# Kernel optimization log

Hardware: AMD Instinct MI355X
Metric: run time of the kernel (lower is better)

Reference implementation:

```python
import jax, jax.numpy as jnp
import numpy as np

N, E, G = 25000, 50000, 1000   # nodes, edges, graphs
NP, EP = 25, 50                # nodes/edges per graph
D = 64                         # node_out_feats


def setup_inputs() -> dict:
    key = jax.random.key(0)
    ks = jax.random.split(key, 32)
    rng = np.random.RandomState(0)
    # edges stay within their graph (molecular batch structure)
    base = np.repeat(np.arange(G), EP) * NP
    src = jnp.asarray(base + rng.randint(0, NP, E), dtype=jnp.int32)
    dst = jnp.asarray(base + rng.randint(0, NP, E), dtype=jnp.int32)
    graph_ids = jnp.repeat(jnp.arange(G, dtype=jnp.int32), NP)

    def p(i, shape, s=0.05):
        return (jax.random.normal(ks[i], shape, jnp.float32) * s)

    return dict(
        n_feats=jax.random.normal(ks[0], (N, 74), jnp.float32),
        e_feats=jax.random.normal(ks[1], (E, 12), jnp.float32),
        src=src, dst=dst, graph_ids=graph_ids,
        # project_node_feats: Linear(74,64)+ReLU
        proj_W=p(2, (74, D)), proj_b=jnp.zeros((D,), jnp.float32),
        # NNConv edge network: Linear(12,64)+ReLU+Linear(64,64*64)
        eW1=p(3, (12, D)), eb1=jnp.zeros((D,), jnp.float32),
        eW2=p(4, (D, D * D)), eb2=jnp.zeros((D * D,), jnp.float32),
        conv_b=jnp.zeros((D,), jnp.float32),
        # GRU (1 layer, gates r,z,n) stored transposed: x @ W
        gru_Wi=p(5, (D, 3 * D)), gru_Wh=p(6, (D, 3 * D)),
        gru_bi=jnp.zeros((3 * D,), jnp.float32), gru_bh=jnp.zeros((3 * D,), jnp.float32),
        # Set2Set LSTM: 3 layers, input 2D (layer0) / D, hidden D, gates i,f,g,o
        lWi0=p(7, (2 * D, 4 * D)), lWh0=p(8, (D, 4 * D)), lb0=jnp.zeros((4 * D,), jnp.float32),
        lWi1=p(9, (D, 4 * D)), lWh1=p(10, (D, 4 * D)), lb1=jnp.zeros((4 * D,), jnp.float32),
        lWi2=p(11, (D, 4 * D)), lWh2=p(12, (D, 4 * D)), lb2=jnp.zeros((4 * D,), jnp.float32),
        # predict hidden: Linear(128,64)+ReLU, then head fc: Linear(64,1)
        pW=p(13, (2 * D, D)), pb=jnp.zeros((D,), jnp.float32),
        fW=p(14, (D, 1)), fb=jnp.zeros((1,), jnp.float32),
    )


def reference(n_feats, e_feats, src, dst, graph_ids,
              proj_W, proj_b, eW1, eb1, eW2, eb2, conv_b,
              gru_Wi, gru_Wh, gru_bi, gru_bh,
              lWi0, lWh0, lb0, lWi1, lWh1, lb1, lWi2, lWh2, lb2,
              pW, pb, fW, fb):
    # --- MPNNGNN ---
    h = jax.nn.relu(n_feats @ proj_W + proj_b)                      # (N, D)
    W_e = (jax.nn.relu(e_feats @ eW1 + eb1) @ eW2 + eb2).reshape(E, D, D)
    g = h                                                            # GRU hidden init = node feats
    for _ in range(3):
        msg = jnp.einsum('ei,eio->eo', h[src], W_e)                  # per-edge message
        m = jax.nn.relu(jax.ops.segment_sum(msg, dst, num_segments=N) + conv_b)
        gi = m @ gru_Wi + gru_bi
        gh = g @ gru_Wh + gru_bh
        ir, iz, inn = jnp.split(gi, 3, -1)
        hr, hz, hn = jnp.split(gh, 3, -1)
        r = jax.nn.sigmoid(ir + hr)
        z = jax.nn.sigmoid(iz + hz)
        nn_ = jnp.tanh(inn + r * hn)
        g = (1.0 - z) * nn_ + z * g
        h = g
    # --- Set2Set readout (3 iters, 3-layer LSTM) ---
    Wis, Whs, bs = [lWi0, lWi1, lWi2], [lWh0, lWh1, lWh2], [lb0, lb1, lb2]
    hs = [jnp.zeros((G, D), h.dtype) for _ in range(3)]
    cs = [jnp.zeros((G, D), h.dtype) for _ in range(3)]
    q_star = jnp.zeros((G, 2 * D), h.dtype)
    for _ in range(3):
        x = q_star
        for l in range(3):
            gates = x @ Wis[l] + hs[l] @ Whs[l] + bs[l]
            i, f, gg, o = jnp.split(gates, 4, -1)
            cs[l] = jax.nn.sigmoid(f) * cs[l] + jax.nn.sigmoid(i) * jnp.tanh(gg)
            hs[l] = jax.nn.sigmoid(o) * jnp.tanh(cs[l])
            x = hs[l]
        q = x                                                        # (G, D)
        e = jnp.sum(h * q[graph_ids], -1)                            # (N,)
        e = e - jax.ops.segment_max(e, graph_ids, num_segments=G)[graph_ids]
        ex = jnp.exp(e)
        alpha = ex / jax.ops.segment_sum(ex, graph_ids, num_segments=G)[graph_ids]
        rdt = jax.ops.segment_sum(alpha[:, None] * h, graph_ids, num_segments=G)
        q_star = jnp.concatenate([q, rdt], -1)                       # (G, 2D)
    # --- predict hidden + head ---
    graph_feats = jax.nn.relu(q_star @ pW + pb)                      # (G, D)
    return jax.nn.sigmoid(graph_feats @ fW + fb)[:, 0]               # (G,)
```

## Files before the change

kernel.cpp:

```cpp
#include <hip/hip_runtime.h>
#include <math.h>

__device__ __forceinline__ float sigf(float x) { return 1.f / (1.f + expf(-x)); }

using half8v = __attribute__((ext_vector_type(8))) _Float16;
using f32x4  = __attribute__((ext_vector_type(4))) float;

__device__ __forceinline__ unsigned short f2h(float x) {
    union { _Float16 h; unsigned short u; } c; c.h = (_Float16)x; return c.u;
}
__device__ __forceinline__ half8v u2h(uint4 v) {
    union { uint4 u; half8v h; } c; c.u = v; return c.h;
}

template<int K, int MODE>
__global__ __launch_bounds__(256, 4)
void rowmat_relu_t(const float* __restrict__ in, const float* __restrict__ W,
                   const float* __restrict__ b, float* __restrict__ out32,
                   _Float16* __restrict__ out16, int R)
{
    __shared__ float Wl[K * 64];
    __shared__ float rowsS[32 * K];

    const int tid  = threadIdx.x;
    const int row0 = blockIdx.x * 32;

    for (int i = tid; i < K * 64; i += 256)
        Wl[i] = W[i];
    const int lim = (R - row0 >= 32 ? 32 : (R - row0)) * K;
    for (int i = tid; i < 32 * K; i += 256)
        rowsS[i] = (i < lim) ? in[(size_t)row0 * K + i] : 0.f;
    __syncthreads();

    const int wave = tid >> 6, lane = tid & 63;
    const float bv = b[lane];

    float acc[8];
    #pragma unroll
    for (int rr = 0; rr < 8; ++rr) acc[rr] = bv;

    #pragma unroll 2
    for (int k = 0; k < K; ++k) {
        const float wv = Wl[k * 64 + lane];
        #pragma unroll
        for (int rr = 0; rr < 8; ++rr)
            acc[rr] = fmaf(rowsS[(wave * 8 + rr) * K + k], wv, acc[rr]);
    }

    #pragma unroll
    for (int rr = 0; rr < 8; ++rr) {
        const int row = row0 + wave * 8 + rr;
        if (row < R) {
            const float v = fmaxf(acc[rr], 0.f);
            if (MODE == 0) out32[(size_t)row * 64 + lane] = v;
            out16[(size_t)row * 64 + lane] = (_Float16)v;
        }
    }
}

__global__ __launch_bounds__(256)
void prep_w_kernel(const float* __restrict__ eW2, const float* __restrict__ eb2,
                   unsigned short* __restrict__ w_staged)
{
    int slot = blockIdx.x * 256 + threadIdx.x;
    if (slot >= 65 * 512) return;
    int kc   = slot >> 9;
    int s    = slot & 511;
    int sub  = s >> 6, lane = s & 63;
    int wn   = sub >> 2, tn = (sub >> 1) & 1, ks = sub & 1;
    int kg   = lane >> 4, l15 = lane & 15;
    int o    = wn * 32 + tn * 16 + l15;
    int seg  = kg + ks * 4;
    int j0   = kc * 64 + seg * 8;
    unsigned int packed[4];
    #pragma unroll
    for (int p = 0; p < 4; ++p) {
        int j = j0 + p * 2;
        float v0 = (j     < 4096) ? eW2[(size_t)j * 64 + o]       : eb2[(size_t)(j - 4096) * 64 + o];
        float v1 = (j + 1 < 4096) ? eW2[(size_t)(j + 1) * 64 + o] : eb2[(size_t)(j + 1 - 4096) * 64 + o];
        packed[p] = (unsigned int)f2h(v0) | ((unsigned int)f2h(v1) << 16);
    }
    uint4 st = {packed[0], packed[1], packed[2], packed[3]};
    ((uint4*)w_staged)[slot] = st;
}

__global__ __launch_bounds__(256)
void prep_gruw_kernel(const float* __restrict__ Wi, const float* __restrict__ Wh,
                      _Float16* __restrict__ WiT, _Float16* __restrict__ WhT)
{
    int idx = blockIdx.x * 256 + threadIdx.x;
    if (idx >= 2 * 12288) return;
    const float* W = (idx < 12288) ? Wi : Wh;
    _Float16*    O = (idx < 12288) ? WiT : WhT;
    int r = idx & 12287;
    int n = r >> 6, k = r & 63;
    O[n * 64 + k] = (_Float16)W[(size_t)k * 192 + n];
}

__global__ __launch_bounds__(256)
void prep_s2sw_kernel(const float* __restrict__ lWi0, const float* __restrict__ lWh0,
                      const float* __restrict__ lWi1, const float* __restrict__ lWh1,
                      const float* __restrict__ lWi2, const float* __restrict__ lWh2,
                      _Float16* __restrict__ WB0, _Float16* __restrict__ WB1,
                      _Float16* __restrict__ WB2)
{
    int idx = blockIdx.x * 256 + threadIdx.x;
    if (idx < 49152) {
        int k = idx >> 8, n = idx & 255;
        float v = (k < 128) ? lWi0[(size_t)k * 256 + n] : lWh0[(size_t)(k - 128) * 256 + n];
        WB0[((k >> 3) * 2048) + n * 8 + (k & 7)] = (_Float16)v;
    } else if (idx < 81920) {
        int r = idx - 49152;
        int k = r >> 8, n = r & 255;
        float v = (k < 64) ? lWi1[(size_t)k * 256 + n] : lWh1[(size_t)(k - 64) * 256 + n];
        WB1[((k >> 3) * 2048) + n * 8 + (k & 7)] = (_Float16)v;
    } else if (idx < 114688) {
        int r = idx - 81920;
        int k = r >> 8, n = r & 255;
        float v = (k < 64) ? lWi2[(size_t)k * 256 + n] : lWh2[(size_t)(k - 64) * 256 + n];
        WB2[((k >> 3) * 2048) + n * 8 + (k & 7)] = (_Float16)v;
    }
}

__global__ __launch_bounds__(512, 4)
void msg_mfma_kernel(const _Float16* __restrict__ t16, const _Float16* __restrict__ h16,
                     const int* __restrict__ src, const int* __restrict__ dst,
                     const unsigned short* __restrict__ w_staged,
                     float* __restrict__ msum, int E)
{
    __shared__ _Float16 tS[64 * 134];

    const int tid  = threadIdx.x;
    const int lane = tid & 63;
    const int wave = tid >> 6;
    const int wn   = wave & 1;
    const int wm   = wave >> 1;
    const int e0   = blockIdx.x * 128;

    #pragma unroll
    for (int p = 0; p < 2; ++p) {
        int slot = tid + p * 512;
        int e = slot >> 3, k0 = (slot & 7) * 8;
        int ee = e0 + e;
        half8v tv8 = (half8v)(_Float16)0.f;
        if (ee < E) tv8 = ((const half8v*)(t16 + (size_t)ee * 64))[slot & 7];
        #pragma unroll
        for (int j = 0; j < 8; ++j)
            tS[(k0 + j) * 134 + e] = tv8[j];
    }

    const int l15 = lane & 15;
    const int kg  = lane >> 4;

    half8v Hh[2][2];
    #pragma unroll
    for (int tm = 0; tm < 2; ++tm) {
        const int edge = e0 + wm * 32 + tm * 16 + l15;
        const int sidx = (edge < E) ? src[edge] : 0;
        const half8v* hp = (const half8v*)(h16 + (size_t)sidx * 64);
        Hh[tm][0] = hp[kg];
        Hh[tm][1] = hp[kg + 4];
    }

    const uint4* W4  = (const uint4*)w_staged;
    const int    wb  = wn * 256 + lane;

    uint4 S0a, S0b, S0c, S0d, S1a, S1b, S1c, S1d;
    uint4 S2a, S2b, S2c, S2d, S3a, S3b, S3c, S3d;

#define LOADC(A, B, C, D, cc)                                         \
    { size_t off = (size_t)(cc) * 512 + wb;                           \
      A = W4[off]; B = W4[off + 64]; C = W4[off + 128]; D = W4[off + 192]; }

#define COMP(A, B, C, D, TV0, TV1)                                            \
    { half8v af00 = Hh[0][0] * (TV0), af01 = Hh[0][1] * (TV0);                \
      half8v af10 = Hh[1][0] * (TV1), af11 = Hh[1][1] * (TV1);                \
      half8v b00 = u2h(A), b01 = u2h(B), b10 = u2h(C), b11 = u2h(D);          \
      acc00 = __builtin_amdgcn_mfma_f32_16x16x32_f16(af00, b00, acc00, 0,0,0);\
      acc01 = __builtin_amdgcn_mfma_f32_16x16x32_f16(af00, b10, acc01, 0,0,0);\
      acc10 = __builtin_amdgcn_mfma_f32_16x16x32_f16(af10, b00, acc10, 0,0,0);\
      acc11 = __builtin_amdgcn_mfma_f32_16x16x32_f16(af10, b10, acc11, 0,0,0);\
      acc00 = __builtin_amdgcn_mfma_f32_16x16x32_f16(af01, b01, acc00, 0,0,0);\
      acc01 = __builtin_amdgcn_mfma_f32_16x16x32_f16(af01, b11, acc01, 0,0,0);\
      acc10 = __builtin_amdgcn_mfma_f32_16x16x32_f16(af11, b01, acc10, 0,0,0);\
      acc11 = __builtin_amdgcn_mfma_f32_16x16x32_f16(af11, b11, acc11, 0,0,0); }

    LOADC(S0a, S0b, S0c, S0d, 0)
    LOADC(S1a, S1b, S1c, S1d, 1)
    LOADC(S2a, S2b, S2c, S2d, 2)
    LOADC(S3a, S3b, S3c, S3d, 3)

    f32x4 acc00, acc01, acc10, acc11;
    #pragma unroll
    for (int j = 0; j < 4; ++j) { acc00[j] = 0.f; acc01[j] = 0.f; acc10[j] = 0.f; acc11[j] = 0.f; }

    __syncthreads();

    const int tvb0 = wm * 32 + l15, tvb1 = wm * 32 + 16 + l15;

    for (int c = 0; c < 64; c += 4) {
        _Float16 ta0 = tS[(c + 0) * 134 + tvb0], tb0 = tS[(c + 0) * 134 + tvb1];
        _Float16 ta1 = tS[(c + 1) * 134 + tvb0], tb1 = tS[(c + 1) * 134 + tvb1];
        _Float16 ta2 = tS[(c + 2) * 134 + tvb0], tb2 = tS[(c + 2) * 134 + tvb1];
        _Float16 ta3 = tS[(c + 3) * 134 + tvb0], tb3 = tS[(c + 3) * 134 + tvb1];

        COMP(S0a, S0b, S0c, S0d, ta0, tb0)
        if (c + 4 <= 64) LOADC(S0a, S0b, S0c, S0d, c + 4)
        COMP(S1a, S1b, S1c, S1d, ta1, tb1)
        if (c + 5 <= 64) LOADC(S1a, S1b, S1c, S1d, c + 5)
        COMP(S2a, S2b, S2c, S2d, ta2, tb2)
        if (c + 6 <= 64) LOADC(S2a, S2b, S2c, S2d, c + 6)
        COMP(S3a, S3b, S3c, S3d, ta3, tb3)
        if (c + 7 <= 64) LOADC(S3a, S3b, S3c, S3d, c + 7)
    }
    {
        const _Float16 one = (_Float16)1.0f;
        COMP(S0a, S0b, S0c, S0d, one, one)
    }
#undef LOADC
#undef COMP

    f32x4 acc[2][2] = {{acc00, acc01}, {acc10, acc11}};
    #pragma unroll
    for (int tm = 0; tm < 2; ++tm) {
        #pragma unroll
        for (int j = 0; j < 4; ++j) {
            const int edge = e0 + wm * 32 + tm * 16 + kg * 4 + j;
            if (edge >= E) continue;
            const int d = dst[edge];
            #pragma unroll
            for (int tn = 0; tn < 2; ++tn)
                atomicAdd(&msum[(size_t)d * 64 + wn * 32 + tn * 16 + l15], acc[tm][tn][j]);
        }
    }
}

__global__ __launch_bounds__(256, 2)
void gru_mfma_kernel(const float* __restrict__ msum, float* __restrict__ h,
                     _Float16* __restrict__ h16,
                     const _Float16* __restrict__ WiT, const _Float16* __restrict__ WhT,
                     const float* __restrict__ bi, const float* __restrict__ bh,
                     const float* __restrict__ conv_b, int N)
{
    __shared__ _Float16 BtI[192 * 72];
    __shared__ _Float16 BtH[192 * 72];
    __shared__ _Float16 Am[64 * 72];
    __shared__ _Float16 Ah[64 * 72];

    const int tid  = threadIdx.x;
    const int lane = tid & 63;
    const int wave = tid >> 6;
    const int m0   = wave * 16;
    const int row0 = blockIdx.x * 64;

    #pragma unroll
    for (int p = 0; p < 6; ++p) {
        int slot = tid + p * 256;
        int n = slot >> 3, k0 = (slot & 7) * 8;
        uint4 vi = ((const uint4*)WiT)[slot];
        uint4 vh = ((const uint4*)WhT)[slot];
        *(uint4*)&BtI[n * 72 + k0] = vi;
        *(uint4*)&BtH[n * 72 + k0] = vh;
    }
    #pragma unroll
    for (int p = 0; p < 4; ++p) {
        int idx = tid + p * 256;
        int r = idx >> 4, k4 = (idx & 15) * 4;
        int row = row0 + r;
        float4 mv = make_float4(0.f, 0.f, 0.f, 0.f);
        if (row < N) mv = *(const float4*)&msum[(size_t)row * 64 + k4];
        float4 cb = *(const float4*)&conv_b[k4];
        union { _Float16 hx[4]; uint2 u2; } pk;
        pk.hx[0] = (_Float16)fmaxf(mv.x + cb.x, 0.f);
        pk.hx[1] = (_Float16)fmaxf(mv.y + cb.y, 0.f);
        pk.hx[2] = (_Float16)fmaxf(mv.z + cb.z, 0.f);
        pk.hx[3] = (_Float16)fmaxf(mv.w + cb.w, 0.f);
        *(uint2*)&Am[r * 72 + k4] = pk.u2;
    }
    #pragma unroll
    for (int p = 0; p < 2; ++p) {
        int idx = tid + p * 256;
        int r = idx >> 3, k0 = (idx & 7) * 8;
        int row = row0 + r;
        uint4 v = {0u, 0u, 0u, 0u};
        if (row < N) v = *(const uint4*)&h16[(size_t)row * 64 + k0];
        *(uint4*)&Ah[r * 72 + k0] = v;
    }
    __syncthreads();

    const int l15 = lane & 15;

    f32x4 acc_i[12], acc_h[12];
    #pragma unroll
    for (int nt = 0; nt < 12; ++nt) {
        #pragma unroll
        for (int j = 0; j < 4; ++j) { acc_i[nt][j] = 0.f; acc_h[nt][j] = 0.f; }
    }

    #pragma unroll
    for (int ks = 0; ks < 2; ++ks) {
        const int ka = ks * 32 + (lane >> 4) * 8;
        half8v am = *(const half8v*)&Am[(m0 + l15) * 72 + ka];
        half8v ah = *(const half8v*)&Ah[(m0 + l15) * 72 + ka];
        #pragma unroll
        for (int nt = 0; nt < 12; ++nt) {
            half8v b_i = *(const half8v*)&BtI[(nt * 16 + l15) * 72 + ka];
            half8v b_h = *(const half8v*)&BtH[(nt * 16 + l15) * 72 + ka];
            acc_i[nt] = __builtin_amdgcn_mfma_f32_16x16x32_f16(am, b_i, acc_i[nt], 0, 0, 0);
            acc_h[nt] = __builtin_amdgcn_mfma_f32_16x16x32_f16(ah, b_h, acc_h[nt], 0, 0, 0);
        }
    }

    const int rgrp = lane >> 4;
    #pragma unroll
    for (int nt0 = 0; nt0 < 4; ++nt0) {
        const int c = nt0 * 16 + l15;
        const float bir = bi[c],        bhr = bh[c];
        const float biz = bi[64 + c],   bhz = bh[64 + c];
        const float bin = bi[128 + c],  bhn = bh[128 + c];
        #pragma unroll
        for (int j = 0; j < 4; ++j) {
            const int row = row0 + m0 + rgrp * 4 + j;
            if (row >= N) continue;
            float rg = sigf(acc_i[nt0][j]      + bir + acc_h[nt0][j]      + bhr);
            float zg = sigf(acc_i[4 + nt0][j]  + biz + acc_h[4 + nt0][j]  + bhz);
            float ng = tanhf(acc_i[8 + nt0][j] + bin + rg * (acc_h[8 + nt0][j] + bhn));
            float hold = h[(size_t)row * 64 + c];
            float hv = (1.f - zg) * ng + zg * hold;
            h[(size_t)row * 64 + c]   = hv;
            h16[(size_t)row * 64 + c] = (_Float16)hv;
        }
    }
}

__device__ __forceinline__ float gate_dot8(const _Float16* __restrict__ WB,
                                           int tid, const float* __restrict__ xs,
                                           int nblk)
{
    float a0 = 0.f, a1 = 0.f, a2 = 0.f, a3 = 0.f;
    #pragma unroll 4
    for (int b = 0; b < nblk; ++b) {
        half8v w = *(const half8v*)(WB + (size_t)b * 2048 + tid * 8);
        float4 xa = *(const float4*)&xs[b * 8];
        float4 xb = *(const float4*)&xs[b * 8 + 4];
        a0 = fmaf((float)w[0], xa.x, a0);
        a1 = fmaf((float)w[1], xa.y, a1);
        a2 = fmaf((float)w[2], xa.z, a2);
        a3 = fmaf((float)w[3], xa.w, a3);
        a0 = fmaf((float)w[4], xb.x, a0);
        a1 = fmaf((float)w[5], xb.y, a1);
        a2 = fmaf((float)w[6], xb.z, a2);
        a3 = fmaf((float)w[7], xb.w, a3);
    }
    return (a0 + a1) + (a2 + a3);
}

__global__ __launch_bounds__(256)
void set2set_kernel(const float* __restrict__ h,
                    const _Float16* __restrict__ WB0, const _Float16* __restrict__ WB1,
                    const _Float16* __restrict__ WB2,
                    const float* __restrict__ lb0, const float* __restrict__ lb1,
                    const float* __restrict__ lb2,
                    const float* __restrict__ pW, const float* __restrict__ pb,
                    const float* __restrict__ fW, const float* __restrict__ fb,
                    float* __restrict__ out)
{
    const int g   = blockIdx.x;
    const int tid = threadIdx.x;

    __shared__ float hl[25 * 65];
    __shared__ float hs[3][64], cs[3][64];
    __shared__ float qstar[128];
    __shared__ __align__(16) float xs[192];
    __shared__ float gates[256];
    __shared__ float als[32];

    for (int idx = tid; idx < 25 * 64; idx += 256) {
        int n = idx >> 6, d = idx & 63;
        hl[n * 65 + d] = h[((size_t)g * 25 + n) * 64 + d];
    }
    if (tid < 128) qstar[tid] = 0.f;
    if (tid < 64) {
        #pragma unroll
        for (int l = 0; l < 3; ++l) { hs[l][tid] = 0.f; cs[l][tid] = 0.f; }
    }
    __syncthreads();

    for (int it = 0; it < 3; ++it) {
        if (tid < 128) xs[tid] = qstar[tid];
        else if (tid < 192) xs[tid] = hs[0][tid - 128];
        __syncthreads();
        gates[tid] = lb0[tid] + gate_dot8(WB0, tid, xs, 24);
        __syncthreads();
        if (tid < 64) {
            float ig = sigf(gates[tid]);
            float fg = sigf(gates[64 + tid]);
            float gg = tanhf(gates[128 + tid]);
            float og = sigf(gates[192 + tid]);
            float cv = fg * cs[0][tid] + ig * gg;
            cs[0][tid] = cv;
            hs[0][tid] = og * tanhf(cv);
        }
        __syncthreads();
        if (tid < 64) xs[tid] = hs[0][tid];
        else if (tid < 128) xs[tid] = hs[1][tid - 64];
        __syncthreads();
        gates[tid] = lb1[tid] + gate_dot8(WB1, tid, xs, 16);
        __syncthreads();
        if (tid < 64) {
            float ig = sigf(gates[tid]);
            float fg = sigf(gates[64 + tid]);
            float gg = tanhf(gates[128 + tid]);
            float og = sigf(gates[192 + tid]);
            float cv = fg * cs[1][tid] + ig * gg;
            cs[1][tid] = cv;
            hs[1][tid] = og * tanhf(cv);
        }
        __syncthreads();
        if (tid < 64) xs[tid] = hs[1][tid];
        else if (tid < 128) xs[tid] = hs[2][tid - 64];
        __syncthreads();
        gates[tid] = lb2[tid] + gate_dot8(WB2, tid, xs, 16);
        __syncthreads();
        if (tid < 64) {
            float ig = sigf(gates[tid]);
            float fg = sigf(gates[64 + tid]);
            float gg = tanhf(gates[128 + tid]);
            float og = sigf(gates[192 + tid]);
            float cv = fg * cs[2][tid] + ig * gg;
            cs[2][tid] = cv;
            hs[2][tid] = og * tanhf(cv);
        }
        __syncthreads();
        float ev = -1e30f;
        if (tid < 25) {
            float acc = 0.f;
            for (int d = 0; d < 64; ++d)
                acc = fmaf(hl[tid * 65 + d], hs[2][d], acc);
            ev = acc;
        }
        if (tid < 64) {
            float mx = ev;
            #pragma unroll
            for (int off = 16; off; off >>= 1) mx = fmaxf(mx, __shfl_xor(mx, off, 32));
            float ex = (tid < 25) ? expf(ev - mx) : 0.f;
            float sm = ex;
            #pragma unroll
            for (int off = 16; off; off >>= 1) sm += __shfl_xor(sm, off, 32);
            if (tid < 25) als[tid] = ex / sm;
        }
        __syncthreads();
        if (tid < 64) {
            float rdt = 0.f;
            #pragma unroll
            for (int n = 0; n < 25; ++n) rdt = fmaf(als[n], hl[n * 65 + tid], rdt);
            qstar[tid]      = hs[2][tid];
            qstar[64 + tid] = rdt;
        }
        __syncthreads();
    }

    if (tid < 64) {
        float acc = pb[tid];
        #pragma unroll 8
        for (int k = 0; k < 128; ++k)
            acc = fmaf(qstar[k], pW[(size_t)k * 64 + tid], acc);
        float part = fmaxf(acc, 0.f) * fW[tid];
        #pragma unroll
        for (int off = 32; off; off >>= 1) part += __shfl_xor(part, off, 64);
        if (tid == 0) out[g] = 1.f / (1.f + expf(-(part + fb[0])));
    }
}

extern "C" void kernel_launch(void* const* d_in, const int* in_sizes, int n_in,
                              void* d_out, int out_size, void* d_ws, size_t ws_size,
                              hipStream_t stream)
{
    const float* n_feats = (const float*)d_in[0];
    const float* e_feats = (const float*)d_in[1];
    const int*   src     = (const int*)d_in[2];
    const int*   dst     = (const int*)d_in[3];
    const float* proj_W  = (const float*)d_in[5];
    const float* proj_b  = (const float*)d_in[6];
    const float* eW1     = (const float*)d_in[7];
    const float* eb1     = (const float*)d_in[8];
    const float* eW2     = (const float*)d_in[9];
    const float* eb2     = (const float*)d_in[10];
    const float* conv_b  = (const float*)d_in[11];
    const float* gWi     = (const float*)d_in[12];
    const float* gWh     = (const float*)d_in[13];
    const float* gbi     = (const float*)d_in[14];
    const float* gbh     = (const float*)d_in[15];
    const float* lWi0    = (const float*)d_in[16];
    const float* lWh0    = (const float*)d_in[17];
    const float* lb0     = (const float*)d_in[18];
    const float* lWi1    = (const float*)d_in[19];
    const float* lWh1    = (const float*)d_in[20];
    const float* lb1     = (const float*)d_in[21];
    const float* lWi2    = (const float*)d_in[22];
    const float* lWh2    = (const float*)d_in[23];
    const float* lb2     = (const float*)d_in[24];
    const float* pW      = (const float*)d_in[25];
    const float* pb      = (const float*)d_in[26];
    const float* fW      = (const float*)d_in[27];
    const float* fb      = (const float*)d_in[28];

    const int N = in_sizes[0] / 74;
    const int E = in_sizes[1] / 12;
    const int G = out_size;

    float* ws   = (float*)d_ws;
    float* h    = ws;
    float* msum = h + (size_t)N * 64;
    _Float16* h16 = (_Float16*)(msum + (size_t)N * 64);
    _Float16* t16 = h16 + (size_t)N * 64;
    unsigned short* w_staged = (unsigned short*)(t16 + (size_t)E * 64);
    _Float16* WiT = (_Float16*)(w_staged + 65 * 4096);
    _Float16* WhT = WiT + 12288;
    _Float16* WB0 = WhT + 12288;
    _Float16* WB1 = WB0 + 49152;
    _Float16* WB2 = WB1 + 32768;

    prep_w_kernel<<<130, 256, 0, stream>>>(eW2, eb2, w_staged);
    prep_gruw_kernel<<<96, 256, 0, stream>>>(gWi, gWh, WiT, WhT);
    prep_s2sw_kernel<<<448, 256, 0, stream>>>(lWi0, lWh0, lWi1, lWh1, lWi2, lWh2,
                                              WB0, WB1, WB2);

    rowmat_relu_t<74, 0><<<(N + 31) / 32, 256, 0, stream>>>(n_feats, proj_W, proj_b, h, h16, N);
    rowmat_relu_t<12, 1><<<(E + 31) / 32, 256, 0, stream>>>(e_feats, eW1, eb1, nullptr, t16, E);

    for (int it = 0; it < 3; ++it) {
        hipMemsetAsync(msum, 0, (size_t)N * 64 * sizeof(float), stream);
        msg_mfma_kernel<<<(E + 127) / 128, 512, 0, stream>>>(t16, h16, src, dst, w_staged, msum, E);
        gru_mfma_kernel<<<(N + 63) / 64, 256, 0, stream>>>(msum, h, h16, WiT, WhT,
                                                           gbi, gbh, conv_b, N);
    }

    set2set_kernel<<<G, 256, 0, stream>>>(h, WB0, WB1, WB2, lb0, lb1, lb2,
                                          pW, pb, fW, fb, (float*)d_out);
}
```

Baseline: 267.9 us.

## Split message kernel reduction dimension across two blocks per edge tile

Each 128-edge tile of the NNConv message kernel is now processed by two blocks. Each block covers half of the 64 edge-hidden channels, and the block with the upper half also adds the bias chunk. This doubles the grid (about 391 to 782 blocks) and halves shared memory per block, which should improve occupancy and latency hiding on the MI355X. The cost is doubled atomicAdd traffic into msum and redundant gathers of the h16 source rows in both blocks.

```diff
diff --git a/kernel.cpp b/kernel.cpp
--- a/kernel.cpp
+++ b/kernel.cpp
@@ -128,25 +128,26 @@
                      const unsigned short* __restrict__ w_staged,
                      float* __restrict__ msum, int E)
 {
-    __shared__ _Float16 tS[64 * 134];
-
-    const int tid  = threadIdx.x;
-    const int lane = tid & 63;
-    const int wave = tid >> 6;
-    const int wn   = wave & 1;
-    const int wm   = wave >> 1;
-    const int e0   = blockIdx.x * 128;
-
-    #pragma unroll
-    for (int p = 0; p < 2; ++p) {
-        int slot = tid + p * 512;
-        int e = slot >> 3, k0 = (slot & 7) * 8;
+    __shared__ _Float16 tS[32 * 134];
+
+    const int tid    = threadIdx.x;
+    const int lane   = tid & 63;
+    const int wave   = tid >> 6;
+    const int wn     = wave & 1;
+    const int wm     = wave >> 1;
+    const int e0     = (blockIdx.x >> 1) * 128;
+    const int ksplit = blockIdx.x & 1;
+    const int cbase  = ksplit * 32;
+    const int cend   = cbase + 32;
+
+    {
+        int e = tid >> 2, g = tid & 3;
         int ee = e0 + e;
         half8v tv8 = (half8v)(_Float16)0.f;
-        if (ee < E) tv8 = ((const half8v*)(t16 + (size_t)ee * 64))[slot & 7];
+        if (ee < E) tv8 = ((const half8v*)(t16 + (size_t)ee * 64))[(cbase >> 3) + g];
         #pragma unroll
         for (int j = 0; j < 8; ++j)
-            tS[(k0 + j) * 134 + e] = tv8[j];
+            tS[(g * 8 + j) * 134 + e] = tv8[j];
     }
 
     const int l15 = lane & 15;
@@ -185,10 +186,10 @@
       acc10 = __builtin_amdgcn_mfma_f32_16x16x32_f16(af11, b01, acc10, 0,0,0);\
       acc11 = __builtin_amdgcn_mfma_f32_16x16x32_f16(af11, b11, acc11, 0,0,0); }
 
-    LOADC(S0a, S0b, S0c, S0d, 0)
-    LOADC(S1a, S1b, S1c, S1d, 1)
-    LOADC(S2a, S2b, S2c, S2d, 2)
-    LOADC(S3a, S3b, S3c, S3d, 3)
+    LOADC(S0a, S0b, S0c, S0d, cbase + 0)
+    LOADC(S1a, S1b, S1c, S1d, cbase + 1)
+    LOADC(S2a, S2b, S2c, S2d, cbase + 2)
+    LOADC(S3a, S3b, S3c, S3d, cbase + 3)
 
     f32x4 acc00, acc01, acc10, acc11;
     #pragma unroll
@@ -198,22 +199,24 @@
 
     const int tvb0 = wm * 32 + l15, tvb1 = wm * 32 + 16 + l15;
 
-    for (int c = 0; c < 64; c += 4) {
-        _Float16 ta0 = tS[(c + 0) * 134 + tvb0], tb0 = tS[(c + 0) * 134 + tvb1];
-        _Float16 ta1 = tS[(c + 1) * 134 + tvb0], tb1 = tS[(c + 1) * 134 + tvb1];
-        _Float16 ta2 = tS[(c + 2) * 134 + tvb0], tb2 = tS[(c + 2) * 134 + tvb1];
-        _Float16 ta3 = tS[(c + 3) * 134 + tvb0], tb3 = tS[(c + 3) * 134 + tvb1];
+    for (int c = cbase; c < cend; c += 4) {
+        const int cl = c - cbase;
+        _Float16 ta0 = tS[(cl + 0) * 134 + tvb0], tb0 = tS[(cl + 0) * 134 + tvb1];
+        _Float16 ta1 = tS[(cl + 1) * 134 + tvb0], tb1 = tS[(cl + 1) * 134 + tvb1];
+        _Float16 ta2 = tS[(cl + 2) * 134 + tvb0], tb2 = tS[(cl + 2) * 134 + tvb1];
+        _Float16 ta3 = tS[(cl + 3) * 134 + tvb0], tb3 = tS[(cl + 3) * 134 + tvb1];
 
         COMP(S0a, S0b, S0c, S0d, ta0, tb0)
-        if (c + 4 <= 64) LOADC(S0a, S0b, S0c, S0d, c + 4)
+        if (c + 4 < cend) { LOADC(S0a, S0b, S0c, S0d, c + 4) }
+        else if (ksplit)  { LOADC(S0a, S0b, S0c, S0d, 64) }
         COMP(S1a, S1b, S1c, S1d, ta1, tb1)
-        if (c + 5 <= 64) LOADC(S1a, S1b, S1c, S1d, c + 5)
+        if (c + 5 < cend) LOADC(S1a, S1b, S1c, S1d, c + 5)
         COMP(S2a, S2b, S2c, S2d, ta2, tb2)
-        if (c + 6 <= 64) LOADC(S2a, S2b, S2c, S2d, c + 6)
+        if (c + 6 < cend) LOADC(S2a, S2b, S2c, S2d, c + 6)
         COMP(S3a, S3b, S3c, S3d, ta3, tb3)
-        if (c + 7 <= 64) LOADC(S3a, S3b, S3c, S3d, c + 7)
-    }
-    {
+        if (c + 7 < cend) LOADC(S3a, S3b, S3c, S3d, c + 7)
+    }
+    if (ksplit) {
         const _Float16 one = (_Float16)1.0f;
         COMP(S0a, S0b, S0c, S0d, one, one)
     }
@@ -529,9 +532,10 @@
     rowmat_relu_t<74, 0><<<(N + 31) / 32, 256, 0, stream>>>(n_feats, proj_W, proj_b, h, h16, N);
     rowmat_relu_t<12, 1><<<(E + 31) / 32, 256, 0, stream>>>(e_feats, eW1, eb1, nullptr, t16, E);
 
+    const int msg_blocks = ((E + 127) / 128) * 2;
     for (int it = 0; it < 3; ++it) {
         hipMemsetAsync(msum, 0, (size_t)N * 64 * sizeof(float), stream);
-        msg_mfma_kernel<<<(E + 127) / 128, 512, 0, stream>>>(t16, h16, src, dst, w_staged, msum, E);
+        msg_mfma_kernel<<<msg_blocks, 512, 0, stream>>>(t16, h16, src, dst, w_staged, msum, E);
         gru_mfma_kernel<<<(N + 63) / 64, 256, 0, stream>>>(msum, h, h16, WiT, WhT,
                                                            gbi, gbh, conv_b, N);
     }
```

After: 305.6 us. +14.1%, slower.
